# Kernel tuning notes

Hardware: AMD Instinct MI355X
Metric: run time of the kernel (lower is better)

## Reference

```python
import jax, jax.numpy as jnp
import numpy as np

B, S, D = 2, 2048, 2048
H, KV = 16, 4
HD = D // H          # 128
QPK = H // KV        # queries per kv head


def setup_inputs() -> dict:
    key = jax.random.key(0)
    ks = jax.random.split(key, 8)
    x = jax.random.normal(ks[0], (B, S, D), jnp.float32)
    mask = jnp.zeros((1, 1, S, S), jnp.float32)  # unused (causal flash path)
    # RoPE tables: theta=10000, shape (S, HD//2)
    inv_freq = 1.0 / (10000.0 ** (jnp.arange(0, HD, 2, dtype=jnp.float32) / HD))
    freqs = jnp.outer(jnp.arange(S, dtype=jnp.float32), inv_freq)
    freqs_cos, freqs_sin = jnp.cos(freqs), jnp.sin(freqs)
    sc = 0.02
    Wq = jax.random.normal(ks[1], (D, H * HD), jnp.float32) * sc
    bq = jnp.zeros((H * HD,), jnp.float32)
    Wk = jax.random.normal(ks[2], (D, KV * HD), jnp.float32) * sc
    bk = jnp.zeros((KV * HD,), jnp.float32)
    Wv = jax.random.normal(ks[3], (D, KV * HD), jnp.float32) * sc
    bv = jnp.zeros((KV * HD,), jnp.float32)
    Wo = jax.random.normal(ks[4], (D, D), jnp.float32) * sc  # bias=False
    return dict(x=x, mask=mask, freqs_cos=freqs_cos, freqs_sin=freqs_sin,
                Wq=Wq, bq=bq, Wk=Wk, bk=bk, Wv=Wv, bv=bv, Wo=Wo)


def _rope(t, cos, sin):
    # t: [B, S, nH, HD]; interleaved-pair rotation as in apply_rope
    tr = t.reshape(t.shape[:-1] + (-1, 2))
    r, i = tr[..., 0], tr[..., 1]
    c = cos[None, :, None, :]
    s = sin[None, :, None, :]
    out = jnp.stack([r * c - i * s, r * s + i * c], axis=-1)
    return out.reshape(t.shape)


def reference(x, mask, freqs_cos, freqs_sin, Wq, bq, Wk, bk, Wv, bv, Wo):
    b, s, d = x.shape
    q = (x @ Wq + bq).reshape(b, s, H, HD)
    k = (x @ Wk + bk).reshape(b, s, KV, HD)
    v = (x @ Wv + bv).reshape(b, s, KV, HD)
    cos, sin = freqs_cos[:s], freqs_sin[:s]
    q = _rope(q, cos, sin)
    k = _rope(k, cos, sin)
    # GQA: repeat_interleave kv heads to match query heads
    k = jnp.repeat(k, QPK, axis=2)
    v = jnp.repeat(v, QPK, axis=2)
    q = q.transpose(0, 2, 1, 3)  # [B, H, S, HD]
    k = k.transpose(0, 2, 1, 3)
    v = v.transpose(0, 2, 1, 3)
    scores = jnp.einsum('bhqd,bhkd->bhqk', q, k) / jnp.sqrt(jnp.float32(HD))
    causal = jnp.tril(jnp.ones((s, s), bool))
    scores = jnp.where(causal[None, None], scores, jnp.finfo(scores.dtype).min)
    attn = jax.nn.softmax(scores, axis=-1)
    out = jnp.einsum('bhqk,bhkd->bhqd', attn, v)
    out = out.transpose(0, 2, 1, 3).reshape(b, s, d)
    return out @ Wo
```

## Files before the change

kernel.cpp:

```cpp
#include <hip/hip_runtime.h>


#define B_  2
#define S_  2048
#define D_  2048
#define H_  16
#define KV_ 4
#define HD_ 128
#define NQKV 3072

typedef unsigned short ushort_t;
typedef __attribute__((ext_vector_type(8))) __bf16 bf16x8;
typedef __attribute__((ext_vector_type(4))) float  f32x4;

__device__ __forceinline__ ushort_t f2bf(float f) {
    unsigned u = __float_as_uint(f);
    u += 0x7FFFu + ((u >> 16) & 1u);
    return (ushort_t)(u >> 16);
}
__device__ __forceinline__ float bf2f(ushort_t h) {
    return __uint_as_float(((unsigned)h) << 16);
}

__device__ __forceinline__ void g2l16(const void* g, void* l) {
    __builtin_amdgcn_global_load_lds(
        (const __attribute__((address_space(1))) unsigned int*)g,
        (__attribute__((address_space(3))) unsigned int*)l, 16, 0, 0);
}


__global__ __launch_bounds__(256) void k_prep(
    const float* __restrict__ x,  ushort_t* __restrict__ xb,
    const float* __restrict__ Wq, const float* __restrict__ Wk,
    const float* __restrict__ Wv, const float* __restrict__ Wo,
    ushort_t* __restrict__ Wt, ushort_t* __restrict__ Wot,
    const float* __restrict__ bq, const float* __restrict__ bk,
    const float* __restrict__ bv, float* __restrict__ bb) {
    __shared__ float tile[32][33];
    int id = blockIdx.x, t = threadIdx.x;
    if (id < 8192) {
        int i = id * 256 + t;
        float4 v = ((const float4*)x)[i];
        ushort4 o;
        o.x = f2bf(v.x); o.y = f2bf(v.y); o.z = f2bf(v.z); o.w = f2bf(v.w);
        ((ushort4*)xb)[i] = o;
        return;
    }
    const float* src; ushort_t* dst; int C, bid;
    if (id < 12288)      { src = Wq; dst = Wt;                       C = 2048; bid = id - 8192;  }
    else if (id < 13312) { src = Wk; dst = Wt + (size_t)2048 * 2048; C = 512;  bid = id - 12288; }
    else if (id < 14336) { src = Wv; dst = Wt + (size_t)2560 * 2048; C = 512;  bid = id - 13312; }
    else if (id < 18432) { src = Wo; dst = Wot;                      C = 2048; bid = id - 14336; }
    else {
        int i = (id - 18432) * 256 + t;
        if (i < 3072)
            bb[i] = (i < 2048) ? bq[i] : (i < 2560) ? bk[i - 2048] : bv[i - 2560];
        return;
    }
    const int R = 2048;
    int nbc = C >> 5;
    int c0 = (bid % nbc) * 32, r0 = (bid / nbc) * 32;
    int tx = t & 31, ty = t >> 5;
    for (int i = ty; i < 32; i += 8)
        tile[i][tx] = src[(size_t)(r0 + i) * C + c0 + tx];
    __syncthreads();
    for (int i = ty; i < 32; i += 8)
        dst[(size_t)(c0 + i) * R + r0 + tx] = f2bf(tile[tx][i]);
}


__global__ __launch_bounds__(256, 3) void k_gemm(const ushort_t* __restrict__ A,
                                                 const ushort_t* __restrict__ Bt,
                                                 void* __restrict__ Cp,
                                                 const float* __restrict__ bias,
                                                 const float* __restrict__ fc,
                                                 const float* __restrict__ fs,
                                                 int M, int N, int K, int out_bf16) {
    __shared__ __align__(16) ushort_t As[128 * 64];
    __shared__ __align__(16) ushort_t Bs[128 * 64];
    int t = threadIdx.x;
    int w = t >> 6, lane = t & 63, quad = lane >> 4, l16 = lane & 15;
    int L = blockIdx.x;
    int mper = (M >> 7) >> 3;
    int xcd = L & 7, j = L >> 3;
    int m0 = (xcd * mper + (j % mper)) * 128;
    int n0 = (j / mper) * 128;
    int wm = (w >> 1) * 64, wn = (w & 1) * 64;
    f32x4 acc[4][4] = {};

    int srow = lane >> 3;
    int sgs  = (lane & 7) ^ srow;
    const ushort_t* Ag = A  + (size_t)(m0 + w * 32 + srow) * K + sgs * 8;
    const ushort_t* Bg = Bt + (size_t)(n0 + w * 32 + srow) * K + sgs * 8;
    char* AsW = (char*)As + w * 4096;
    char* BsW = (char*)Bs + w * 4096;
    int rsw = (l16 & 7);

    for (int k0 = 0; k0 < K; k0 += 64) {
        __syncthreads();
#pragma unroll
        for (int p = 0; p < 4; p++) {
            g2l16(Ag + (size_t)(p * 8) * K + k0, AsW + p * 1024);
            g2l16(Bg + (size_t)(p * 8) * K + k0, BsW + p * 1024);
        }
        __syncthreads();
#pragma unroll
        for (int kc = 0; kc < 2; kc++) {
            int gg = quad + kc * 4;
            bf16x8 af[4], bfr[4];
#pragma unroll
            for (int i = 0; i < 4; i++)
                af[i] = *(const bf16x8*)(As + (wm + i * 16 + l16) * 64 + ((gg ^ rsw) * 8));
#pragma unroll
            for (int j2 = 0; j2 < 4; j2++)
                bfr[j2] = *(const bf16x8*)(Bs + (wn + j2 * 16 + l16) * 64 + ((gg ^ rsw) * 8));
#pragma unroll
            for (int i = 0; i < 4; i++)
#pragma unroll
                for (int j2 = 0; j2 < 4; j2++)
                    acc[i][j2] = __builtin_amdgcn_mfma_f32_16x16x32_bf16(af[i], bfr[j2], acc[i][j2], 0, 0, 0);
        }
    }
#pragma unroll
    for (int i = 0; i < 4; i++) {
        int r = m0 + wm + i * 16 + quad * 4;
#pragma unroll
        for (int j2 = 0; j2 < 4; j2++) {
            int c = n0 + wn + j2 * 16 + l16;
            float bv_ = bias ? bias[c] : 0.f;
#pragma unroll
            for (int jr = 0; jr < 4; jr++) {
                float v = acc[i][j2][jr] + bv_;
                if (fc && c < 2560) {
                    int s  = (r + jr) & (S_ - 1);
                    int dp = (c & 127) >> 1;
                    float cs = fc[s * 64 + dp], sn = fs[s * 64 + dp];
                    float p = __shfl_xor(v, 1);
                    v = (c & 1) ? (v * cs + p * sn) : (v * cs - p * sn);
                }
                if (out_bf16) ((ushort_t*)Cp)[(size_t)(r + jr) * N + c] = f2bf(v);
                else          ((float*)Cp)[(size_t)(r + jr) * N + c] = v;
            }
        }
    }
}


__global__ __launch_bounds__(256) void k_vtrans(const ushort_t* __restrict__ QKV,
                                                ushort_t* __restrict__ Vt) {
    __shared__ ushort_t tile[32][33];
    int s0 = blockIdx.x * 32, d0 = blockIdx.y * 32, bz = blockIdx.z;
    int b = bz >> 2, kv = bz & 3;
    int tx = threadIdx.x, ty = threadIdx.y;
    for (int i = ty; i < 32; i += 8)
        tile[i][tx] = QKV[(size_t)(b * S_ + s0 + i) * NQKV + 2560 + kv * HD_ + d0 + tx];
    __syncthreads();
    for (int i = ty; i < 32; i += 8)
        Vt[((size_t)((b * KV_ + kv) * HD_ + d0 + i)) * S_ + s0 + tx] = tile[tx][i];
}


__global__ __launch_bounds__(512, 4) void k_flash(const ushort_t* __restrict__ QKV,
                                                  const ushort_t* __restrict__ Vt,
                                                  ushort_t* __restrict__ AO) {
    __shared__ __align__(16) ushort_t Ks[2 * 8192];
    __shared__ __align__(16) ushort_t Vs[2 * 8192];
    __shared__ __align__(16) ushort_t Ps[8 * 16 * 64];
    int h = blockIdx.y, b = blockIdx.z;
    int qt = b ? ((int)gridDim.x - 1 - (int)blockIdx.x) : (int)blockIdx.x;
    int kvh = h >> 2;
    int t = threadIdx.x, w = t >> 6, lane = t & 63, quad = lane >> 4, l16 = lane & 15;
    int qrow0 = qt * 128 + w * 16;
    const float SOFT = 0.08838834764831845f * 1.4426950408889634f;

    bf16x8 aq[4];
    {
        const ushort_t* qb = QKV + (size_t)(b * S_ + qrow0 + l16) * NQKV + h * HD_ + quad * 8;
#pragma unroll
        for (int kc = 0; kc < 4; kc++) aq[kc] = *(const bf16x8*)(qb + kc * 32);
    }
    bf16x8 vone;
#pragma unroll
    for (int i = 0; i < 8; i++) vone[i] = (__bf16)1.0f;

    f32x4 o[8] = {};
    f32x4 ol = {};
    ushort_t* Psw = Ps + w * 16 * 64;
    int gsw = (l16 >> 1) & 3;

    const ushort_t* kgb = QKV + (size_t)(b * S_) * NQKV + 2048 + kvh * HD_;
    const ushort_t* vgb = Vt + ((size_t)(b * KV_ + kvh) * HD_) * S_;

    int sr, sgs; char *sK0, *sV0;
    if (t < 256) {
        sr = t >> 2; sgs = (t & 3) ^ ((sr >> 1) & 3);
        sK0 = (char*)Ks + (t >> 6) * 1024;
        sV0 = nullptr;
    } else {
        int u = t - 256;
        sr = u >> 2; sgs = (u & 3) ^ ((sr >> 1) & 3);
        sV0 = (char*)Vs + ((t - 256) >> 6) * 1024;
        sK0 = nullptr;
    }

#define STAGE(KT, BUF)                                                          \
    do {                                                                        \
        if (t < 256) {                                                          \
            const ushort_t* kg = kgb + (size_t)((KT) * 64 + sr) * NQKV + sgs * 8; \
            char* KsW = sK0 + (BUF) * 16384;                                    \
            _Pragma("unroll")                                                   \
            for (int p = 0; p < 4; p++) g2l16(kg + p * 32, KsW + p * 4096);     \
        } else {                                                                \
            const ushort_t* vg = vgb + (KT) * 64 + sgs * 8 + (size_t)sr * S_;   \
            char* VsW = sV0 + (BUF) * 16384;                                    \
            _Pragma("unroll")                                                   \
            for (int p = 0; p < 4; p++)                                         \
                g2l16(vg + (size_t)((p & 1) * 64) * S_ + (p >> 1) * 32, VsW + p * 4096); \
        }                                                                       \
    } while (0)

    int ktmax = 2 * qt + 1;
    STAGE(0, 0);
    __syncthreads();

    for (int kt = 0; kt <= ktmax; kt++) {
        int cur = kt & 1;
        if (kt < ktmax) STAGE(kt + 1, cur ^ 1);

        if (kt * 64 <= qrow0 + 15) {
            const ushort_t* Kc = Ks + cur * 8192;
            const ushort_t* Vc = Vs + cur * 8192;
            f32x4 sacc[4] = {};
#pragma unroll
            for (int kc = 0; kc < 4; kc++)
#pragma unroll
                for (int nb = 0; nb < 4; nb++) {
                    bf16x8 bk = *(const bf16x8*)(Kc + kc * 2048 + (nb * 16 + l16) * 32 + ((quad ^ gsw) * 8));
                    sacc[nb] = __builtin_amdgcn_mfma_f32_16x16x32_bf16(aq[kc], bk, sacc[nb], 0, 0, 0);
                }
            if (kt * 64 + 63 > qrow0) {
#pragma unroll
                for (int nb = 0; nb < 4; nb++)
#pragma unroll
                    for (int jr = 0; jr < 4; jr++) {
                        int kcol = kt * 64 + nb * 16 + l16;
                        int qr = qrow0 + quad * 4 + jr;
                        if (kcol > qr) sacc[nb][jr] = -1e30f;
                    }
            }
#pragma unroll
            for (int nb = 0; nb < 4; nb++)
#pragma unroll
                for (int jr = 0; jr < 4; jr++)
                    Psw[(quad * 4 + jr) * 64 + nb * 16 + l16] = f2bf(exp2f(sacc[nb][jr] * SOFT));

            asm volatile("s_waitcnt lgkmcnt(0)" ::: "memory");

#pragma unroll
            for (int kc2 = 0; kc2 < 2; kc2++) {
                bf16x8 ap = *(const bf16x8*)(Psw + l16 * 64 + kc2 * 32 + quad * 8);
                ol = __builtin_amdgcn_mfma_f32_16x16x32_bf16(ap, vone, ol, 0, 0, 0);
#pragma unroll
                for (int db = 0; db < 8; db++) {
                    bf16x8 bv = *(const bf16x8*)(Vc + kc2 * 4096 + (db * 16 + l16) * 32 + ((quad ^ gsw) * 8));
                    o[db] = __builtin_amdgcn_mfma_f32_16x16x32_bf16(ap, bv, o[db], 0, 0, 0);
                }
            }
        }
        __syncthreads();
    }
#undef STAGE

#pragma unroll
    for (int jr = 0; jr < 4; jr++) {
        float inv = 1.0f / ol[jr];
        size_t rbase = (size_t)(b * S_ + qrow0 + quad * 4 + jr) * D_ + h * HD_;
#pragma unroll
        for (int db = 0; db < 8; db++)
            AO[rbase + db * 16 + l16] = f2bf(o[db][jr] * inv);
    }
}


extern "C" void kernel_launch(void* const* d_in, const int* in_sizes, int n_in,
                              void* d_out, int out_size, void* d_ws, size_t ws_size,
                              hipStream_t stream) {
    const float* x  = (const float*)d_in[0];
    const float* fc = (const float*)d_in[2];
    const float* fs = (const float*)d_in[3];
    const float* Wq = (const float*)d_in[4];
    const float* bq = (const float*)d_in[5];
    const float* Wk = (const float*)d_in[6];
    const float* bk = (const float*)d_in[7];
    const float* Wv = (const float*)d_in[8];
    const float* bv = (const float*)d_in[9];
    const float* Wo = (const float*)d_in[10];

    char* ws = (char*)d_ws;
    ushort_t* xb  = (ushort_t*)(ws);
    ushort_t* Wt  = (ushort_t*)(ws + 16777216);
    ushort_t* Wot = (ushort_t*)(ws + 29360128);
    float*    bb  = (float*)   (ws + 37748736);
    ushort_t* QKV = (ushort_t*)(ws + 37761024);
    ushort_t* Vt  = Wt;
    ushort_t* AO  = xb;
    float* out = (float*)d_out;

    k_prep<<<18444, 256, 0, stream>>>(x, xb, Wq, Wk, Wv, Wo, Wt, Wot, bq, bk, bv, bb);
    k_gemm<<<768, 256, 0, stream>>>(xb, Wt, QKV, bb, fc, fs, 4096, 3072, 2048, 1);
    k_vtrans<<<dim3(64, 4, 8), dim3(32, 8), 0, stream>>>(QKV, Vt);
    k_flash<<<dim3(16, 16, 2), 512, 0, stream>>>(QKV, Vt, AO);
    k_gemm<<<512, 256, 0, stream>>>(AO, Wot, out, nullptr, nullptr, nullptr,
                                    4096, 2048, 2048, 0);
}
```

Measured before the change: 323.3 us.

## Fuse V transpose into QKV GEMM epilogue and widen output GEMM K-tile

The QKV projection epilogue now writes the V columns straight into the transposed Vt layout as packed 4-element stores, so the separate k_vtrans kernel and its extra read and write of V are gone. The QK buffer shrinks to a 2560-column stride and Vt gets its own workspace region. The GEMM becomes templated on its K-tile size, and the output projection uses BK=128, which doubles shared memory per block and may reduce occupancy.

```diff
diff --git a/kernel.cpp b/kernel.cpp
--- a/kernel.cpp
+++ b/kernel.cpp
@@ -7,7 +7,7 @@
 #define H_  16
 #define KV_ 4
 #define HD_ 128
-#define NQKV 3072
+#define NQK 2560
 
 typedef unsigned short ushort_t;
 typedef __attribute__((ext_vector_type(8))) __bf16 bf16x8;
@@ -69,15 +69,20 @@
 }
 
 
+template<int BK>
 __global__ __launch_bounds__(256, 3) void k_gemm(const ushort_t* __restrict__ A,
                                                  const ushort_t* __restrict__ Bt,
                                                  void* __restrict__ Cp,
                                                  const float* __restrict__ bias,
                                                  const float* __restrict__ fc,
                                                  const float* __restrict__ fs,
+                                                 ushort_t* __restrict__ Vt,
                                                  int M, int N, int K, int out_bf16) {
-    __shared__ __align__(16) ushort_t As[128 * 64];
-    __shared__ __align__(16) ushort_t Bs[128 * 64];
+    constexpr int GPR    = BK / 8;
+    constexpr int RPR    = 64 / GPR;
+    constexpr int ROUNDS = 32 / RPR;
+    __shared__ __align__(16) ushort_t As[128 * BK];
+    __shared__ __align__(16) ushort_t Bs[128 * BK];
     int t = threadIdx.x;
     int w = t >> 6, lane = t & 63, quad = lane >> 4, l16 = lane & 15;
     int L = blockIdx.x;
@@ -88,32 +93,32 @@
     int wm = (w >> 1) * 64, wn = (w & 1) * 64;
     f32x4 acc[4][4] = {};
 
-    int srow = lane >> 3;
-    int sgs  = (lane & 7) ^ srow;
-    const ushort_t* Ag = A  + (size_t)(m0 + w * 32 + srow) * K + sgs * 8;
-    const ushort_t* Bg = Bt + (size_t)(n0 + w * 32 + srow) * K + sgs * 8;
-    char* AsW = (char*)As + w * 4096;
-    char* BsW = (char*)Bs + w * 4096;
+    int rlo = lane / GPR;
+    int gsl = lane & (GPR - 1);
+    const ushort_t* Ag = A  + (size_t)(m0 + w * 32) * K;
+    const ushort_t* Bg = Bt + (size_t)(n0 + w * 32) * K;
     int rsw = (l16 & 7);
 
-    for (int k0 = 0; k0 < K; k0 += 64) {
+    for (int k0 = 0; k0 < K; k0 += BK) {
         __syncthreads();
 #pragma unroll
-        for (int p = 0; p < 4; p++) {
-            g2l16(Ag + (size_t)(p * 8) * K + k0, AsW + p * 1024);
-            g2l16(Bg + (size_t)(p * 8) * K + k0, BsW + p * 1024);
+        for (int p = 0; p < ROUNDS; p++) {
+            int row = p * RPR + rlo;
+            int gs = gsl ^ (row & 7);
+            g2l16(Ag + (size_t)row * K + k0 + gs * 8, (char*)As + (w * 32 + p * RPR) * 2 * BK);
+            g2l16(Bg + (size_t)row * K + k0 + gs * 8, (char*)Bs + (w * 32 + p * RPR) * 2 * BK);
         }
         __syncthreads();
 #pragma unroll
-        for (int kc = 0; kc < 2; kc++) {
+        for (int kc = 0; kc < BK / 32; kc++) {
             int gg = quad + kc * 4;
             bf16x8 af[4], bfr[4];
 #pragma unroll
             for (int i = 0; i < 4; i++)
-                af[i] = *(const bf16x8*)(As + (wm + i * 16 + l16) * 64 + ((gg ^ rsw) * 8));
+                af[i] = *(const bf16x8*)(As + (wm + i * 16 + l16) * BK + ((gg ^ rsw) * 8));
 #pragma unroll
             for (int j2 = 0; j2 < 4; j2++)
-                bfr[j2] = *(const bf16x8*)(Bs + (wn + j2 * 16 + l16) * 64 + ((gg ^ rsw) * 8));
+                bfr[j2] = *(const bf16x8*)(Bs + (wn + j2 * 16 + l16) * BK + ((gg ^ rsw) * 8));
 #pragma unroll
             for (int i = 0; i < 4; i++)
 #pragma unroll
@@ -121,6 +126,7 @@
                     acc[i][j2] = __builtin_amdgcn_mfma_f32_16x16x32_bf16(af[i], bfr[j2], acc[i][j2], 0, 0, 0);
         }
     }
+    int ostride = fc ? NQK : N;
 #pragma unroll
     for (int i = 0; i < 4; i++) {
         int r = m0 + wm + i * 16 + quad * 4;
@@ -128,39 +134,36 @@
         for (int j2 = 0; j2 < 4; j2++) {
             int c = n0 + wn + j2 * 16 + l16;
             float bv_ = bias ? bias[c] : 0.f;
+            if (fc && c >= 2560) {
+                ushort4 pack;
+                pack.x = f2bf(acc[i][j2][0] + bv_);
+                pack.y = f2bf(acc[i][j2][1] + bv_);
+                pack.z = f2bf(acc[i][j2][2] + bv_);
+                pack.w = f2bf(acc[i][j2][3] + bv_);
+                int kv = (c - 2560) >> 7, d = (c - 2560) & 127;
+                int b = r >> 11, s0 = r & (S_ - 1);
+                *(ushort4*)&Vt[(((size_t)b * KV_ + kv) * HD_ + d) * S_ + s0] = pack;
+                continue;
+            }
 #pragma unroll
             for (int jr = 0; jr < 4; jr++) {
                 float v = acc[i][j2][jr] + bv_;
-                if (fc && c < 2560) {
+                if (fc) {
                     int s  = (r + jr) & (S_ - 1);
                     int dp = (c & 127) >> 1;
                     float cs = fc[s * 64 + dp], sn = fs[s * 64 + dp];
                     float p = __shfl_xor(v, 1);
                     v = (c & 1) ? (v * cs + p * sn) : (v * cs - p * sn);
                 }
-                if (out_bf16) ((ushort_t*)Cp)[(size_t)(r + jr) * N + c] = f2bf(v);
-                else          ((float*)Cp)[(size_t)(r + jr) * N + c] = v;
+                if (out_bf16) ((ushort_t*)Cp)[(size_t)(r + jr) * ostride + c] = f2bf(v);
+                else          ((float*)Cp)[(size_t)(r + jr) * ostride + c] = v;
             }
         }
     }
 }
 
 
-__global__ __launch_bounds__(256) void k_vtrans(const ushort_t* __restrict__ QKV,
-                                                ushort_t* __restrict__ Vt) {
-    __shared__ ushort_t tile[32][33];
-    int s0 = blockIdx.x * 32, d0 = blockIdx.y * 32, bz = blockIdx.z;
-    int b = bz >> 2, kv = bz & 3;
-    int tx = threadIdx.x, ty = threadIdx.y;
-    for (int i = ty; i < 32; i += 8)
-        tile[i][tx] = QKV[(size_t)(b * S_ + s0 + i) * NQKV + 2560 + kv * HD_ + d0 + tx];
-    __syncthreads();
-    for (int i = ty; i < 32; i += 8)
-        Vt[((size_t)((b * KV_ + kv) * HD_ + d0 + i)) * S_ + s0 + tx] = tile[tx][i];
-}
-
-
-__global__ __launch_bounds__(512, 4) void k_flash(const ushort_t* __restrict__ QKV,
+__global__ __launch_bounds__(512, 4) void k_flash(const ushort_t* __restrict__ QK,
                                                   const ushort_t* __restrict__ Vt,
                                                   ushort_t* __restrict__ AO) {
     __shared__ __align__(16) ushort_t Ks[2 * 8192];
@@ -175,7 +178,7 @@
 
     bf16x8 aq[4];
     {
-        const ushort_t* qb = QKV + (size_t)(b * S_ + qrow0 + l16) * NQKV + h * HD_ + quad * 8;
+        const ushort_t* qb = QK + (size_t)(b * S_ + qrow0 + l16) * NQK + h * HD_ + quad * 8;
 #pragma unroll
         for (int kc = 0; kc < 4; kc++) aq[kc] = *(const bf16x8*)(qb + kc * 32);
     }
@@ -188,7 +191,7 @@
     ushort_t* Psw = Ps + w * 16 * 64;
     int gsw = (l16 >> 1) & 3;
 
-    const ushort_t* kgb = QKV + (size_t)(b * S_) * NQKV + 2048 + kvh * HD_;
+    const ushort_t* kgb = QK + (size_t)(b * S_) * NQK + 2048 + kvh * HD_;
     const ushort_t* vgb = Vt + ((size_t)(b * KV_ + kvh) * HD_) * S_;
 
     int sr, sgs; char *sK0, *sV0;
@@ -206,7 +209,7 @@
 #define STAGE(KT, BUF)                                                          \
     do {                                                                        \
         if (t < 256) {                                                          \
-            const ushort_t* kg = kgb + (size_t)((KT) * 64 + sr) * NQKV + sgs * 8; \
+            const ushort_t* kg = kgb + (size_t)((KT) * 64 + sr) * NQK + sgs * 8; \
             char* KsW = sK0 + (BUF) * 16384;                                    \
             _Pragma("unroll")                                                   \
             for (int p = 0; p < 4; p++) g2l16(kg + p * 32, KsW + p * 4096);     \
@@ -301,15 +304,14 @@
     ushort_t* Wt  = (ushort_t*)(ws + 16777216);
     ushort_t* Wot = (ushort_t*)(ws + 29360128);
     float*    bb  = (float*)   (ws + 37748736);
-    ushort_t* QKV = (ushort_t*)(ws + 37761024);
-    ushort_t* Vt  = Wt;
+    ushort_t* QK  = (ushort_t*)(ws + 37761024);
+    ushort_t* Vt  = (ushort_t*)(ws + 58732544);
     ushort_t* AO  = xb;
     float* out = (float*)d_out;
 
     k_prep<<<18444, 256, 0, stream>>>(x, xb, Wq, Wk, Wv, Wo, Wt, Wot, bq, bk, bv, bb);
-    k_gemm<<<768, 256, 0, stream>>>(xb, Wt, QKV, bb, fc, fs, 4096, 3072, 2048, 1);
-    k_vtrans<<<dim3(64, 4, 8), dim3(32, 8), 0, stream>>>(QKV, Vt);
-    k_flash<<<dim3(16, 16, 2), 512, 0, stream>>>(QKV, Vt, AO);
-    k_gemm<<<512, 256, 0, stream>>>(AO, Wot, out, nullptr, nullptr, nullptr,
-                                    4096, 2048, 2048, 0);
-}
+    k_gemm<64><<<768, 256, 0, stream>>>(xb, Wt, QK, bb, fc, fs, Vt, 4096, 3072, 2048, 1);
+    k_flash<<<dim3(16, 16, 2), 512, 0, stream>>>(QK, Vt, AO);
+    k_gemm<128><<<512, 256, 0, stream>>>(AO, Wot, out, nullptr, nullptr, nullptr, nullptr,
+                                         4096, 2048, 2048, 0);
+}
```

Result: no change. 321.5 us (-0.6%).
